# Kernel tuning notes

Hardware: AMD Instinct MI355X
Metric: run time of the kernel (lower is better)

## Reference

```python
import jax, jax.numpy as jnp
import numpy as np

NUM_HEADS = 12

def setup_inputs() -> dict:
    key = jax.random.key(0)
    ks = jax.random.split(key, 6)
    B, N, C, P = 16, 785, 768, 48
    return {
        "x": jax.random.normal(ks[0], (B, N, C), jnp.float32),
        "qkv_w": jax.random.normal(ks[1], (3 * C, C), jnp.float32) * 0.02,
        "pos_emb": jax.random.normal(ks[2], (N, N, P), jnp.float32) * 0.02,
        "pos_proj_w": jax.random.normal(ks[3], (NUM_HEADS, P), jnp.float32) * 0.02,
        "proj_w": jax.random.normal(ks[4], (C, C), jnp.float32) * 0.02,
        "proj_b": jnp.zeros((C,), jnp.float32),
    }

def reference(x, qkv_w, pos_emb, pos_proj_w, proj_w, proj_b):
    B, N, C = x.shape
    H = NUM_HEADS
    hd = C // H
    scale = hd ** -0.5
    # qkv projection: [B,N,3C] -> q,k,v each [B,H,N,hd]
    qkv = (x @ qkv_w.T).reshape(B, N, 3, H, hd)
    qkv = jnp.transpose(qkv, (2, 0, 3, 1, 4))
    q, k, v = qkv[0], qkv[1], qkv[2]
    # learned relative-position bias: [H,N,N]
    pos_score = jnp.einsum('nmp,hp->hnm', pos_emb, pos_proj_w)
    # attention scores: scale applied AFTER adding bias (matches original)
    attn = (jnp.einsum('bhnd,bhmd->bhnm', q, k) + pos_score[None]) * scale
    attn = jax.nn.softmax(attn, axis=-1)
    out = jnp.einsum('bhnm,bhmd->bhnd', attn, v)
    out = jnp.transpose(out, (0, 2, 1, 3)).reshape(B, N, C)
    return out @ proj_w.T + proj_b
```

## Files before the change

### kernel.cpp

```cpp
#include <hip/hip_runtime.h>
#include <hip/hip_fp16.h>

#define B_ 16
#define N_ 785
#define C_ 768
#define H_ 12
#define HD_ 64
#define P_ 48
#define M_ (B_*N_)
#define POSW 832
#define VTW  832
#define SLOG2E 0.1803368801111244f

#define OFF_Q   0
#define OFF_K   9646080
#define OFF_VT  19292160
#define OFF_POS 29515776
#define OFF_XF  37353216
#define OFF_AO  OFF_XF
#define OFF_WQ  47085312
#define OFF_WP  48854784

struct __align__(16) Half8 { __half h[8]; };
typedef _Float16 half8_t __attribute__((ext_vector_type(8)));
typedef _Float16 half4_t __attribute__((ext_vector_type(4)));
typedef float f32x4 __attribute__((ext_vector_type(4)));

__device__ __forceinline__ void gl16(const void* g, void* l) {
    __builtin_amdgcn_global_load_lds(
        (const __attribute__((address_space(1))) void*)g,
        (__attribute__((address_space(3))) void*)l, 16, 0, 0);
}

__device__ __forceinline__ int xcd_swz(int o, int nwg) {
    const int q = nwg >> 3, r = nwg & 7;
    const int xcd = o & 7, idx = o >> 3;
    const int base = xcd < r ? xcd * (q + 1) : r * (q + 1) + (xcd - r) * q;
    return base + idx;
}

#define NX4 2411520
#define NQ4 442368
#define NP4 147456
#define NTOT4 (NX4+NQ4+NP4)

__global__ __launch_bounds__(256) void convert_f16(
    const float* __restrict__ x, const float* __restrict__ wq,
    const float* __restrict__ wp, _Float16* __restrict__ xo,
    _Float16* __restrict__ wqo, _Float16* __restrict__ wpo)
{
    int i = blockIdx.x * 256 + threadIdx.x;
    const float4* s; _Float16* d; int o;
    if (i < NX4)            { s = (const float4*)x;  d = xo;  o = i; }
    else if (i < NX4 + NQ4) { s = (const float4*)wq; d = wqo; o = i - NX4; }
    else                    { s = (const float4*)wp; d = wpo; o = i - NX4 - NQ4; }
    float4 v = s[o];
    half4_t h = { (_Float16)v.x, (_Float16)v.y, (_Float16)v.z, (_Float16)v.w };
    *(half4_t*)&d[o * 4] = h;
}

#define QKV_NWG (18 * 99)

__global__ __launch_bounds__(256) void qkv_gemm_mfma(
    const _Float16* __restrict__ A, const _Float16* __restrict__ Bw,
    __half* __restrict__ qh, __half* __restrict__ kh, __half* __restrict__ vth)
{
    __shared__ _Float16 Asl[2][128 * 32];
    __shared__ _Float16 Bsl[2][128 * 32];

    const int t  = threadIdx.x;
    const int w  = t >> 6;
    const int l  = t & 63;
    const int lr = l & 15;
    const int lg = l >> 4;
    const int wm = (w >> 1) * 64;
    const int wn = (w & 1) * 64;

    const int g  = xcd_swz(blockIdx.x, QKV_NWG);
    const int nt = g % 18;
    const int n0 = nt * 128;
    const int m0 = (g / 18) * 128;

    const int f1 = t + 256;
    const int ar0 = t >> 2,  ac0 = (t & 3) * 8;
    const int ar1 = f1 >> 2, ac1 = (f1 & 3) * 8;
    const _Float16* Ag0 = A  + (size_t)(m0 + ar0) * 768 + ac0;
    const _Float16* Ag1 = A  + (size_t)(m0 + ar1) * 768 + ac1;
    const _Float16* Bg0 = Bw + (size_t)(n0 + ar0) * 768 + ac0;
    const _Float16* Bg1 = Bw + (size_t)(n0 + ar1) * 768 + ac1;

    f32x4 acc[4][4];
    #pragma unroll
    for (int i = 0; i < 4; ++i)
        #pragma unroll
        for (int j = 0; j < 4; ++j) acc[i][j] = (f32x4){0.f, 0.f, 0.f, 0.f};

    gl16(Ag0, &Asl[0][t * 8]); gl16(Ag1, &Asl[0][f1 * 8]);
    gl16(Bg0, &Bsl[0][t * 8]); gl16(Bg1, &Bsl[0][f1 * 8]);
    __syncthreads();

    #pragma unroll 2
    for (int it = 0; it < 24; ++it) {
        const int cur = it & 1;
        if (it < 23) {
            const int kn = (it + 1) * 32;
            gl16(Ag0 + kn, &Asl[cur ^ 1][t * 8]); gl16(Ag1 + kn, &Asl[cur ^ 1][f1 * 8]);
            gl16(Bg0 + kn, &Bsl[cur ^ 1][t * 8]); gl16(Bg1 + kn, &Bsl[cur ^ 1][f1 * 8]);
        }
        half8_t af[4], bf[4];
        #pragma unroll
        for (int i = 0; i < 4; ++i)
            af[i] = *(const half8_t*)&Asl[cur][(wm + i * 16 + lr) * 32 + lg * 8];
        #pragma unroll
        for (int j = 0; j < 4; ++j)
            bf[j] = *(const half8_t*)&Bsl[cur][(wn + j * 16 + lr) * 32 + lg * 8];
        __builtin_amdgcn_s_setprio(1);
        #pragma unroll
        for (int i = 0; i < 4; ++i)
            #pragma unroll
            for (int j = 0; j < 4; ++j)
                acc[i][j] = __builtin_amdgcn_mfma_f32_16x16x32_f16(af[i], bf[j], acc[i][j], 0, 0, 0);
        __builtin_amdgcn_s_setprio(0);
        __syncthreads();
    }

    const int tsel  = nt / 6;
    const int nbase = n0 - tsel * 768;
    #pragma unroll
    for (int i = 0; i < 4; ++i) {
        #pragma unroll
        for (int r = 0; r < 4; ++r) {
            const int m = m0 + wm + i * 16 + lg * 4 + r;
            if (m >= M_) continue;
            const int bb = m / N_, nn = m - bb * N_;
            #pragma unroll
            for (int j = 0; j < 4; ++j) {
                const int nsec = nbase + wn + j * 16 + lr;
                const int hh = nsec >> 6, dd = nsec & 63;
                const float v = acc[i][j][r];
                if (tsel == 0)
                    qh[((size_t)(bb * H_ + hh) * N_ + nn) * HD_ + dd] = __float2half(v * SLOG2E);
                else if (tsel == 1)
                    kh[((size_t)(bb * H_ + hh) * N_ + nn) * HD_ + dd] = __float2half(v);
                else
                    vth[((size_t)(bb * H_ + hh) * HD_ + dd) * VTW + nn] = __float2half(v);
            }
        }
    }
}

__global__ __launch_bounds__(256) void pos_kernel(
    const float* __restrict__ pe, const float* __restrict__ pw,
    __half* __restrict__ posh)
{
    __shared__ float W[H_][P_];
    const int t = threadIdx.x;
    for (int i = t; i < H_ * P_; i += 256) W[i / P_][i % P_] = pw[i];
    __syncthreads();
    int nm = blockIdx.x * 256 + t;
    if (nm >= N_ * N_) return;
    float e[48];
    const float4* src = (const float4*)(pe + (size_t)nm * 48);
    #pragma unroll
    for (int i = 0; i < 12; ++i) {
        float4 v = src[i];
        e[4*i] = v.x; e[4*i+1] = v.y; e[4*i+2] = v.z; e[4*i+3] = v.w;
    }
    int n = nm / N_, m = nm - n * N_;
    #pragma unroll
    for (int hh = 0; hh < H_; ++hh) {
        float s = 0.f;
        #pragma unroll
        for (int p = 0; p < 48; ++p) s = fmaf(e[p], W[hh][p], s);
        posh[((size_t)hh * N_ + n) * POSW + m] = __float2half(s * SLOG2E);
    }
}

__global__ __launch_bounds__(256) void attn_mfma(
    const _Float16* __restrict__ qh, const _Float16* __restrict__ kh,
    const _Float16* __restrict__ vt, const _Float16* __restrict__ posh,
    _Float16* __restrict__ aoh)
{
    __shared__ _Float16 Kl[64][72];
    __shared__ _Float16 Vl[64][72];
    __shared__ _Float16 Bl[64][72];

    const int t  = threadIdx.x;
    const int w  = t >> 6;
    const int l  = t & 63;
    const int lr = l & 15;
    const int lg = l >> 4;

    const int g   = blockIdx.x;
    const int b   = g & 15;
    const int grp = g >> 4;
    const int qt  = grp / 12;
    const int h   = grp - qt * 12;
    const int bh  = b * H_ + h;
    const int n0  = qt * 64;

    const int qrow = n0 + w * 16 + lr;
    const int qrc  = qrow < N_ ? qrow : N_ - 1;
    const _Float16* qbase = qh + ((size_t)bh * N_ + qrc) * HD_;
    const half8_t qf0 = *(const half8_t*)(qbase + lg * 8);
    const half8_t qf1 = *(const half8_t*)(qbase + 32 + lg * 8);

    f32x4 O0 = {0.f,0.f,0.f,0.f}, O1 = O0, O2 = O0, O3 = O0;
    float m_run = -1e30f;
    float l_run = 0.f;

    const int srow = t >> 2;
    const int scol = (t & 3) * 16;
    const _Float16* kRow = kh + ((size_t)bh * N_) * HD_ + scol;
    const _Float16* vRow = vt + ((size_t)bh * HD_ + srow) * VTW + scol;
    const _Float16* bRow = posh + ((size_t)h * N_ + (n0 + srow < N_ ? n0 + srow : N_ - 1)) * POSW + scol;

    half8_t rk0, rk1, rv0, rv1, rb0, rb1;
    {
        const int gm = srow < N_ ? srow : N_ - 1;
        const half8_t* ks = (const half8_t*)(kRow + (size_t)gm * HD_);
        rk0 = ks[0]; rk1 = ks[1];
        const half8_t* vs = (const half8_t*)vRow;
        rv0 = vs[0]; rv1 = vs[1];
        const half8_t* bs = (const half8_t*)bRow;
        rb0 = bs[0]; rb1 = bs[1];
    }

    for (int c = 0; c < 13; ++c) {
        *(half8_t*)&Kl[srow][scol]     = rk0;
        *(half8_t*)&Kl[srow][scol + 8] = rk1;
        *(half8_t*)&Vl[srow][scol]     = rv0;
        *(half8_t*)&Vl[srow][scol + 8] = rv1;
        *(half8_t*)&Bl[srow][scol]     = rb0;
        *(half8_t*)&Bl[srow][scol + 8] = rb1;
        __syncthreads();

        if (c < 12) {
            const int m0n = (c + 1) * 64;
            const int gm  = (m0n + srow) < N_ ? (m0n + srow) : N_ - 1;
            const half8_t* ks = (const half8_t*)(kRow + (size_t)gm * HD_);
            rk0 = ks[0]; rk1 = ks[1];
            const half8_t* vs = (const half8_t*)(vRow + m0n);
            rv0 = vs[0]; rv1 = vs[1];
            const half8_t* bs = (const half8_t*)(bRow + m0n);
            rb0 = bs[0]; rb1 = bs[1];
        }

        f32x4 s[4];
        __builtin_amdgcn_s_setprio(1);
        #pragma unroll
        for (int ms = 0; ms < 4; ++ms) {
            half8_t k0 = *(const half8_t*)&Kl[ms * 16 + lr][lg * 8];
            half8_t k1 = *(const half8_t*)&Kl[ms * 16 + lr][32 + lg * 8];
            f32x4 acc = {0.f, 0.f, 0.f, 0.f};
            acc = __builtin_amdgcn_mfma_f32_16x16x32_f16(k0, qf0, acc, 0, 0, 0);
            acc = __builtin_amdgcn_mfma_f32_16x16x32_f16(k1, qf1, acc, 0, 0, 0);
            s[ms] = acc;
        }
        __builtin_amdgcn_s_setprio(0);

        #pragma unroll
        for (int ms = 0; ms < 4; ++ms) {
            half4_t b4 = *(const half4_t*)&Bl[w * 16 + lr][ms * 16 + lg * 4];
            s[ms][0] += (float)b4[0];
            s[ms][1] += (float)b4[1];
            s[ms][2] += (float)b4[2];
            s[ms][3] += (float)b4[3];
        }
        if (c == 12) {
            #pragma unroll
            for (int ms = 0; ms < 4; ++ms)
                #pragma unroll
                for (int r = 0; r < 4; ++r)
                    if (ms * 16 + lg * 4 + r >= 17) s[ms][r] = -1e30f;
        }

        float smax = fmaxf(fmaxf(fmaxf(s[0][0], s[0][1]), fmaxf(s[0][2], s[0][3])),
                           fmaxf(fmaxf(s[1][0], s[1][1]), fmaxf(s[1][2], s[1][3])));
        smax = fmaxf(smax, fmaxf(fmaxf(fmaxf(s[2][0], s[2][1]), fmaxf(s[2][2], s[2][3])),
                                 fmaxf(fmaxf(s[3][0], s[3][1]), fmaxf(s[3][2], s[3][3]))));
        smax = fmaxf(smax, __shfl_xor(smax, 16));
        smax = fmaxf(smax, __shfl_xor(smax, 32));

        if (__any(smax > m_run + 8.f)) {
            const float mn    = fmaxf(m_run, smax);
            const float alpha = exp2f(m_run - mn);
            m_run = mn;
            l_run *= alpha;
            const float a0 = __shfl(alpha, lg * 4 + 0);
            const float a1 = __shfl(alpha, lg * 4 + 1);
            const float a2 = __shfl(alpha, lg * 4 + 2);
            const float a3 = __shfl(alpha, lg * 4 + 3);
            O0[0]*=a0; O0[1]*=a1; O0[2]*=a2; O0[3]*=a3;
            O1[0]*=a0; O1[1]*=a1; O1[2]*=a2; O1[3]*=a3;
            O2[0]*=a0; O2[1]*=a1; O2[2]*=a2; O2[3]*=a3;
            O3[0]*=a0; O3[1]*=a1; O3[2]*=a2; O3[3]*=a3;
        }

        float p[4][4];
        float psum = 0.f;
        #pragma unroll
        for (int ms = 0; ms < 4; ++ms)
            #pragma unroll
            for (int r = 0; r < 4; ++r) {
                p[ms][r] = exp2f(s[ms][r] - m_run);
                psum += p[ms][r];
            }
        psum += __shfl_xor(psum, 16);
        psum += __shfl_xor(psum, 32);
        l_run += psum;

        half8_t pa0 = { (_Float16)p[0][0], (_Float16)p[0][1], (_Float16)p[0][2], (_Float16)p[0][3],
                        (_Float16)p[1][0], (_Float16)p[1][1], (_Float16)p[1][2], (_Float16)p[1][3] };
        half8_t pa1 = { (_Float16)p[2][0], (_Float16)p[2][1], (_Float16)p[2][2], (_Float16)p[2][3],
                        (_Float16)p[3][0], (_Float16)p[3][1], (_Float16)p[3][2], (_Float16)p[3][3] };

        __builtin_amdgcn_s_setprio(1);
        #pragma unroll
        for (int ds = 0; ds < 4; ++ds) {
            const _Float16* vr = &Vl[ds * 16 + lr][0];
            half4_t v00 = *(const half4_t*)&vr[lg * 4];
            half4_t v01 = *(const half4_t*)&vr[16 + lg * 4];
            half4_t v10 = *(const half4_t*)&vr[32 + lg * 4];
            half4_t v11 = *(const half4_t*)&vr[48 + lg * 4];
            half8_t vf0 = __builtin_shufflevector(v00, v01, 0, 1, 2, 3, 4, 5, 6, 7);
            half8_t vf1 = __builtin_shufflevector(v10, v11, 0, 1, 2, 3, 4, 5, 6, 7);
            f32x4& Od = (ds == 0 ? O0 : ds == 1 ? O1 : ds == 2 ? O2 : O3);
            Od = __builtin_amdgcn_mfma_f32_16x16x32_f16(pa0, vf0, Od, 0, 0, 0);
            Od = __builtin_amdgcn_mfma_f32_16x16x32_f16(pa1, vf1, Od, 0, 0, 0);
        }
        __builtin_amdgcn_s_setprio(0);
        __syncthreads();
    }

    const int bb = bh / H_;
    #pragma unroll
    for (int r = 0; r < 4; ++r) {
        const int n = n0 + w * 16 + lg * 4 + r;
        if (n >= N_) continue;
        const float lv  = __shfl(l_run, lg * 4 + r);
        const float inv = 1.f / lv;
        _Float16* dst = aoh + ((size_t)(bb * N_ + n)) * C_ + h * HD_;
        dst[0 * 16 + lr] = (_Float16)(O0[r] * inv);
        dst[1 * 16 + lr] = (_Float16)(O1[r] * inv);
        dst[2 * 16 + lr] = (_Float16)(O2[r] * inv);
        dst[3 * 16 + lr] = (_Float16)(O3[r] * inv);
    }
}

#define PROJ_NWG (6 * 99)

__global__ __launch_bounds__(256) void proj_gemm_mfma(
    const _Float16* __restrict__ A, const _Float16* __restrict__ Bw,
    const float* __restrict__ bias, float* __restrict__ out)
{
    __shared__ _Float16 Asl[2][128 * 32];
    __shared__ _Float16 Bsl[2][128 * 32];

    const int t  = threadIdx.x;
    const int w  = t >> 6;
    const int l  = t & 63;
    const int lr = l & 15;
    const int lg = l >> 4;
    const int wm = (w >> 1) * 64;
    const int wn = (w & 1) * 64;

    const int g  = xcd_swz(blockIdx.x, PROJ_NWG);
    const int n0 = (g % 6) * 128;
    const int m0 = (g / 6) * 128;

    const int f1 = t + 256;
    const int ar0 = t >> 2,  ac0 = (t & 3) * 8;
    const int ar1 = f1 >> 2, ac1 = (f1 & 3) * 8;
    const _Float16* Ag0 = A  + (size_t)(m0 + ar0) * 768 + ac0;
    const _Float16* Ag1 = A  + (size_t)(m0 + ar1) * 768 + ac1;
    const _Float16* Bg0 = Bw + (size_t)(n0 + ar0) * 768 + ac0;
    const _Float16* Bg1 = Bw + (size_t)(n0 + ar1) * 768 + ac1;

    f32x4 acc[4][4];
    #pragma unroll
    for (int i = 0; i < 4; ++i)
        #pragma unroll
        for (int j = 0; j < 4; ++j) acc[i][j] = (f32x4){0.f, 0.f, 0.f, 0.f};

    gl16(Ag0, &Asl[0][t * 8]); gl16(Ag1, &Asl[0][f1 * 8]);
    gl16(Bg0, &Bsl[0][t * 8]); gl16(Bg1, &Bsl[0][f1 * 8]);
    __syncthreads();

    #pragma unroll 2
    for (int it = 0; it < 24; ++it) {
        const int cur = it & 1;
        if (it < 23) {
            const int kn = (it + 1) * 32;
            gl16(Ag0 + kn, &Asl[cur ^ 1][t * 8]); gl16(Ag1 + kn, &Asl[cur ^ 1][f1 * 8]);
            gl16(Bg0 + kn, &Bsl[cur ^ 1][t * 8]); gl16(Bg1 + kn, &Bsl[cur ^ 1][f1 * 8]);
        }
        half8_t af[4], bf[4];
        #pragma unroll
        for (int i = 0; i < 4; ++i)
            af[i] = *(const half8_t*)&Asl[cur][(wm + i * 16 + lr) * 32 + lg * 8];
        #pragma unroll
        for (int j = 0; j < 4; ++j)
            bf[j] = *(const half8_t*)&Bsl[cur][(wn + j * 16 + lr) * 32 + lg * 8];
        __builtin_amdgcn_s_setprio(1);
        #pragma unroll
        for (int i = 0; i < 4; ++i)
            #pragma unroll
            for (int j = 0; j < 4; ++j)
                acc[i][j] = __builtin_amdgcn_mfma_f32_16x16x32_f16(af[i], bf[j], acc[i][j], 0, 0, 0);
        __builtin_amdgcn_s_setprio(0);
        __syncthreads();
    }

    float bj[4];
    #pragma unroll
    for (int j = 0; j < 4; ++j) bj[j] = bias[n0 + wn + j * 16 + lr];
    #pragma unroll
    for (int i = 0; i < 4; ++i) {
        #pragma unroll
        for (int r = 0; r < 4; ++r) {
            const int m = m0 + wm + i * 16 + lg * 4 + r;
            if (m >= M_) continue;
            #pragma unroll
            for (int j = 0; j < 4; ++j) {
                const int n = n0 + wn + j * 16 + lr;
                out[(size_t)m * 768 + n] = acc[i][j][r] + bj[j];
            }
        }
    }
}

extern "C" void kernel_launch(void* const* d_in, const int* in_sizes, int n_in,
                              void* d_out, int out_size, void* d_ws, size_t ws_size,
                              hipStream_t stream)
{
    const float* x     = (const float*)d_in[0];
    const float* qkv_w = (const float*)d_in[1];
    const float* pe    = (const float*)d_in[2];
    const float* pw    = (const float*)d_in[3];
    const float* pjw   = (const float*)d_in[4];
    const float* pjb   = (const float*)d_in[5];
    float* out = (float*)d_out;

    _Float16* wsh  = (_Float16*)d_ws;
    _Float16* qh   = wsh + OFF_Q;
    _Float16* kh   = wsh + OFF_K;
    _Float16* vth  = wsh + OFF_VT;
    _Float16* posh = wsh + OFF_POS;
    _Float16* xf   = wsh + OFF_XF;
    _Float16* aoh  = wsh + OFF_AO;
    _Float16* wqf  = wsh + OFF_WQ;
    _Float16* wpf  = wsh + OFF_WP;

    convert_f16<<<dim3(NTOT4 / 256), 256, 0, stream>>>(x, qkv_w, pjw, xf, wqf, wpf);
    qkv_gemm_mfma<<<dim3(QKV_NWG), 256, 0, stream>>>(
        xf, wqf, (__half*)qh, (__half*)kh, (__half*)vth);
    pos_kernel<<<dim3((N_ * N_ + 255) / 256), 256, 0, stream>>>(pe, pw, (__half*)posh);
    attn_mfma<<<dim3(13 * 12 * 16), 256, 0, stream>>>(qh, kh, vth, posh, aoh);
    proj_gemm_mfma<<<dim3(PROJ_NWG), 256, 0, stream>>>(aoh, wpf, pjb, out);
}
```

Before: 270.1 us.

## Process 128 query rows per attention block to reuse K/V tiles

The attention kernel now assigns two 16-row query groups per wave, so each block covers 128 query rows instead of 64. Each K/V tile staged in shared memory feeds twice as many MFMAs, which halves K/V global traffic and the number of tile loads and barriers. Work-group indices are also remapped through an XCD swizzle so that blocks sharing a (b,h) land together. In exchange, register pressure and shared memory (a larger bias tile) go up, which may lower occupancy. Padding also grows, since the last of the 7 query tiles covers only 17 of its 128 rows.

```diff
diff --git a/kernel.cpp b/kernel.cpp
--- a/kernel.cpp
+++ b/kernel.cpp
@@ -176,6 +176,9 @@
     }
 }
 
+#define NQT 7
+#define ATT_NWG (192 * NQT)
+
 __global__ __launch_bounds__(256) void attn_mfma(
     const _Float16* __restrict__ qh, const _Float16* __restrict__ kh,
     const _Float16* __restrict__ vt, const _Float16* __restrict__ posh,
@@ -183,7 +186,7 @@
 {
     __shared__ _Float16 Kl[64][72];
     __shared__ _Float16 Vl[64][72];
-    __shared__ _Float16 Bl[64][72];
+    __shared__ _Float16 Bl[128][72];
 
     const int t  = threadIdx.x;
     const int w  = t >> 6;
@@ -191,129 +194,161 @@
     const int lr = l & 15;
     const int lg = l >> 4;
 
-    const int g   = blockIdx.x;
-    const int b   = g & 15;
-    const int grp = g >> 4;
-    const int qt  = grp / 12;
-    const int h   = grp - qt * 12;
-    const int bh  = b * H_ + h;
-    const int n0  = qt * 64;
-
-    const int qrow = n0 + w * 16 + lr;
-    const int qrc  = qrow < N_ ? qrow : N_ - 1;
-    const _Float16* qbase = qh + ((size_t)bh * N_ + qrc) * HD_;
-    const half8_t qf0 = *(const half8_t*)(qbase + lg * 8);
-    const half8_t qf1 = *(const half8_t*)(qbase + 32 + lg * 8);
-
-    f32x4 O0 = {0.f,0.f,0.f,0.f}, O1 = O0, O2 = O0, O3 = O0;
-    float m_run = -1e30f;
-    float l_run = 0.f;
+    const int g2   = xcd_swz(blockIdx.x, ATT_NWG);
+    const int qt   = g2 % NQT;
+    const int rest = g2 / NQT;
+    const int b    = rest & 15;
+    const int h    = rest >> 4;
+    const int bh   = b * H_ + h;
+    const int n0   = qt * 128;
+
+    const int qra = min(n0 + w * 32 + lr, N_ - 1);
+    const int qrb = min(n0 + w * 32 + 16 + lr, N_ - 1);
+    const _Float16* qpa = qh + ((size_t)bh * N_ + qra) * HD_;
+    const _Float16* qpb = qh + ((size_t)bh * N_ + qrb) * HD_;
+    const half8_t qf0a = *(const half8_t*)(qpa + lg * 8);
+    const half8_t qf1a = *(const half8_t*)(qpa + 32 + lg * 8);
+    const half8_t qf0b = *(const half8_t*)(qpb + lg * 8);
+    const half8_t qf1b = *(const half8_t*)(qpb + 32 + lg * 8);
+
+    f32x4 Oa0 = {0.f,0.f,0.f,0.f}, Oa1 = Oa0, Oa2 = Oa0, Oa3 = Oa0;
+    f32x4 Ob0 = Oa0, Ob1 = Oa0, Ob2 = Oa0, Ob3 = Oa0;
+    float ma = -1e30f, mb = -1e30f, la = 0.f, lb = 0.f;
 
     const int srow = t >> 2;
     const int scol = (t & 3) * 16;
-    const _Float16* kRow = kh + ((size_t)bh * N_) * HD_ + scol;
-    const _Float16* vRow = vt + ((size_t)bh * HD_ + srow) * VTW + scol;
-    const _Float16* bRow = posh + ((size_t)h * N_ + (n0 + srow < N_ ? n0 + srow : N_ - 1)) * POSW + scol;
-
-    half8_t rk0, rk1, rv0, rv1, rb0, rb1;
+    const _Float16* kRow  = kh + ((size_t)bh * N_) * HD_ + scol;
+    const _Float16* vRow  = vt + ((size_t)bh * HD_ + srow) * VTW + scol;
+    const _Float16* bRow0 = posh + ((size_t)h * N_ + min(n0 + srow,      N_ - 1)) * POSW + scol;
+    const _Float16* bRow1 = posh + ((size_t)h * N_ + min(n0 + 64 + srow, N_ - 1)) * POSW + scol;
+
+    half8_t rk0, rk1, rv0, rv1, rb0, rb1, rb2, rb3;
     {
-        const int gm = srow < N_ ? srow : N_ - 1;
+        const int gm = min(srow, N_ - 1);
         const half8_t* ks = (const half8_t*)(kRow + (size_t)gm * HD_);
         rk0 = ks[0]; rk1 = ks[1];
         const half8_t* vs = (const half8_t*)vRow;
         rv0 = vs[0]; rv1 = vs[1];
-        const half8_t* bs = (const half8_t*)bRow;
-        rb0 = bs[0]; rb1 = bs[1];
+        const half8_t* b0 = (const half8_t*)bRow0;
+        rb0 = b0[0]; rb1 = b0[1];
+        const half8_t* b1 = (const half8_t*)bRow1;
+        rb2 = b1[0]; rb3 = b1[1];
     }
 
     for (int c = 0; c < 13; ++c) {
-        *(half8_t*)&Kl[srow][scol]     = rk0;
-        *(half8_t*)&Kl[srow][scol + 8] = rk1;
-        *(half8_t*)&Vl[srow][scol]     = rv0;
-        *(half8_t*)&Vl[srow][scol + 8] = rv1;
-        *(half8_t*)&Bl[srow][scol]     = rb0;
-        *(half8_t*)&Bl[srow][scol + 8] = rb1;
+        *(half8_t*)&Kl[srow][scol]          = rk0;
+        *(half8_t*)&Kl[srow][scol + 8]      = rk1;
+        *(half8_t*)&Vl[srow][scol]          = rv0;
+        *(half8_t*)&Vl[srow][scol + 8]      = rv1;
+        *(half8_t*)&Bl[srow][scol]          = rb0;
+        *(half8_t*)&Bl[srow][scol + 8]      = rb1;
+        *(half8_t*)&Bl[64 + srow][scol]     = rb2;
+        *(half8_t*)&Bl[64 + srow][scol + 8] = rb3;
         __syncthreads();
 
         if (c < 12) {
             const int m0n = (c + 1) * 64;
-            const int gm  = (m0n + srow) < N_ ? (m0n + srow) : N_ - 1;
+            const int gm  = min(m0n + srow, N_ - 1);
             const half8_t* ks = (const half8_t*)(kRow + (size_t)gm * HD_);
             rk0 = ks[0]; rk1 = ks[1];
             const half8_t* vs = (const half8_t*)(vRow + m0n);
             rv0 = vs[0]; rv1 = vs[1];
-            const half8_t* bs = (const half8_t*)(bRow + m0n);
-            rb0 = bs[0]; rb1 = bs[1];
-        }
-
-        f32x4 s[4];
+            const half8_t* b0 = (const half8_t*)(bRow0 + m0n);
+            rb0 = b0[0]; rb1 = b0[1];
+            const half8_t* b1 = (const half8_t*)(bRow1 + m0n);
+            rb2 = b1[0]; rb3 = b1[1];
+        }
+
+        f32x4 sa[4], sb[4];
         __builtin_amdgcn_s_setprio(1);
         #pragma unroll
         for (int ms = 0; ms < 4; ++ms) {
             half8_t k0 = *(const half8_t*)&Kl[ms * 16 + lr][lg * 8];
             half8_t k1 = *(const half8_t*)&Kl[ms * 16 + lr][32 + lg * 8];
-            f32x4 acc = {0.f, 0.f, 0.f, 0.f};
-            acc = __builtin_amdgcn_mfma_f32_16x16x32_f16(k0, qf0, acc, 0, 0, 0);
-            acc = __builtin_amdgcn_mfma_f32_16x16x32_f16(k1, qf1, acc, 0, 0, 0);
-            s[ms] = acc;
+            f32x4 aa = {0.f, 0.f, 0.f, 0.f};
+            aa = __builtin_amdgcn_mfma_f32_16x16x32_f16(k0, qf0a, aa, 0, 0, 0);
+            aa = __builtin_amdgcn_mfma_f32_16x16x32_f16(k1, qf1a, aa, 0, 0, 0);
+            sa[ms] = aa;
+            f32x4 ab = {0.f, 0.f, 0.f, 0.f};
+            ab = __builtin_amdgcn_mfma_f32_16x16x32_f16(k0, qf0b, ab, 0, 0, 0);
+            ab = __builtin_amdgcn_mfma_f32_16x16x32_f16(k1, qf1b, ab, 0, 0, 0);
+            sb[ms] = ab;
         }
         __builtin_amdgcn_s_setprio(0);
 
         #pragma unroll
         for (int ms = 0; ms < 4; ++ms) {
-            half4_t b4 = *(const half4_t*)&Bl[w * 16 + lr][ms * 16 + lg * 4];
-            s[ms][0] += (float)b4[0];
-            s[ms][1] += (float)b4[1];
-            s[ms][2] += (float)b4[2];
-            s[ms][3] += (float)b4[3];
+            half4_t ba = *(const half4_t*)&Bl[w * 32 + lr][ms * 16 + lg * 4];
+            half4_t bbv = *(const half4_t*)&Bl[w * 32 + 16 + lr][ms * 16 + lg * 4];
+            #pragma unroll
+            for (int r = 0; r < 4; ++r) {
+                sa[ms][r] += (float)ba[r];
+                sb[ms][r] += (float)bbv[r];
+            }
         }
         if (c == 12) {
             #pragma unroll
             for (int ms = 0; ms < 4; ++ms)
                 #pragma unroll
                 for (int r = 0; r < 4; ++r)
-                    if (ms * 16 + lg * 4 + r >= 17) s[ms][r] = -1e30f;
-        }
-
-        float smax = fmaxf(fmaxf(fmaxf(s[0][0], s[0][1]), fmaxf(s[0][2], s[0][3])),
-                           fmaxf(fmaxf(s[1][0], s[1][1]), fmaxf(s[1][2], s[1][3])));
-        smax = fmaxf(smax, fmaxf(fmaxf(fmaxf(s[2][0], s[2][1]), fmaxf(s[2][2], s[2][3])),
-                                 fmaxf(fmaxf(s[3][0], s[3][1]), fmaxf(s[3][2], s[3][3]))));
-        smax = fmaxf(smax, __shfl_xor(smax, 16));
-        smax = fmaxf(smax, __shfl_xor(smax, 32));
-
-        if (__any(smax > m_run + 8.f)) {
-            const float mn    = fmaxf(m_run, smax);
-            const float alpha = exp2f(m_run - mn);
-            m_run = mn;
-            l_run *= alpha;
-            const float a0 = __shfl(alpha, lg * 4 + 0);
-            const float a1 = __shfl(alpha, lg * 4 + 1);
-            const float a2 = __shfl(alpha, lg * 4 + 2);
-            const float a3 = __shfl(alpha, lg * 4 + 3);
-            O0[0]*=a0; O0[1]*=a1; O0[2]*=a2; O0[3]*=a3;
-            O1[0]*=a0; O1[1]*=a1; O1[2]*=a2; O1[3]*=a3;
-            O2[0]*=a0; O2[1]*=a1; O2[2]*=a2; O2[3]*=a3;
-            O3[0]*=a0; O3[1]*=a1; O3[2]*=a2; O3[3]*=a3;
-        }
-
-        float p[4][4];
-        float psum = 0.f;
+                    if (ms * 16 + lg * 4 + r >= 17) { sa[ms][r] = -1e30f; sb[ms][r] = -1e30f; }
+        }
+
+        float sxa = fmaxf(fmaxf(fmaxf(sa[0][0], sa[0][1]), fmaxf(sa[0][2], sa[0][3])),
+                          fmaxf(fmaxf(sa[1][0], sa[1][1]), fmaxf(sa[1][2], sa[1][3])));
+        sxa = fmaxf(sxa, fmaxf(fmaxf(fmaxf(sa[2][0], sa[2][1]), fmaxf(sa[2][2], sa[2][3])),
+                               fmaxf(fmaxf(sa[3][0], sa[3][1]), fmaxf(sa[3][2], sa[3][3]))));
+        sxa = fmaxf(sxa, __shfl_xor(sxa, 16));
+        sxa = fmaxf(sxa, __shfl_xor(sxa, 32));
+        float sxb = fmaxf(fmaxf(fmaxf(sb[0][0], sb[0][1]), fmaxf(sb[0][2], sb[0][3])),
+                          fmaxf(fmaxf(sb[1][0], sb[1][1]), fmaxf(sb[1][2], sb[1][3])));
+        sxb = fmaxf(sxb, fmaxf(fmaxf(fmaxf(sb[2][0], sb[2][1]), fmaxf(sb[2][2], sb[2][3])),
+                               fmaxf(fmaxf(sb[3][0], sb[3][1]), fmaxf(sb[3][2], sb[3][3]))));
+        sxb = fmaxf(sxb, __shfl_xor(sxb, 16));
+        sxb = fmaxf(sxb, __shfl_xor(sxb, 32));
+
+        if (__any(fmaxf(sxa - ma, sxb - mb) > 8.f)) {
+            const float mna = fmaxf(ma, sxa);
+            const float ala = exp2f(ma - mna);
+            ma = mna; la *= ala;
+            const float mnb = fmaxf(mb, sxb);
+            const float alb = exp2f(mb - mnb);
+            mb = mnb; lb *= alb;
+            #pragma unroll
+            for (int r = 0; r < 4; ++r) {
+                const float ar = __shfl(ala, lg * 4 + r);
+                Oa0[r] *= ar; Oa1[r] *= ar; Oa2[r] *= ar; Oa3[r] *= ar;
+                const float br = __shfl(alb, lg * 4 + r);
+                Ob0[r] *= br; Ob1[r] *= br; Ob2[r] *= br; Ob3[r] *= br;
+            }
+        }
+
+        float pa[4][4], pb[4][4];
+        float psa = 0.f, psb = 0.f;
         #pragma unroll
         for (int ms = 0; ms < 4; ++ms)
             #pragma unroll
             for (int r = 0; r < 4; ++r) {
-                p[ms][r] = exp2f(s[ms][r] - m_run);
-                psum += p[ms][r];
+                pa[ms][r] = exp2f(sa[ms][r] - ma);
+                psa += pa[ms][r];
+                pb[ms][r] = exp2f(sb[ms][r] - mb);
+                psb += pb[ms][r];
             }
-        psum += __shfl_xor(psum, 16);
-        psum += __shfl_xor(psum, 32);
-        l_run += psum;
-
-        half8_t pa0 = { (_Float16)p[0][0], (_Float16)p[0][1], (_Float16)p[0][2], (_Float16)p[0][3],
-                        (_Float16)p[1][0], (_Float16)p[1][1], (_Float16)p[1][2], (_Float16)p[1][3] };
-        half8_t pa1 = { (_Float16)p[2][0], (_Float16)p[2][1], (_Float16)p[2][2], (_Float16)p[2][3],
-                        (_Float16)p[3][0], (_Float16)p[3][1], (_Float16)p[3][2], (_Float16)p[3][3] };
+        psa += __shfl_xor(psa, 16);
+        psa += __shfl_xor(psa, 32);
+        la += psa;
+        psb += __shfl_xor(psb, 16);
+        psb += __shfl_xor(psb, 32);
+        lb += psb;
+
+        half8_t paf0 = { (_Float16)pa[0][0], (_Float16)pa[0][1], (_Float16)pa[0][2], (_Float16)pa[0][3],
+                         (_Float16)pa[1][0], (_Float16)pa[1][1], (_Float16)pa[1][2], (_Float16)pa[1][3] };
+        half8_t paf1 = { (_Float16)pa[2][0], (_Float16)pa[2][1], (_Float16)pa[2][2], (_Float16)pa[2][3],
+                         (_Float16)pa[3][0], (_Float16)pa[3][1], (_Float16)pa[3][2], (_Float16)pa[3][3] };
+        half8_t pbf0 = { (_Float16)pb[0][0], (_Float16)pb[0][1], (_Float16)pb[0][2], (_Float16)pb[0][3],
+                         (_Float16)pb[1][0], (_Float16)pb[1][1], (_Float16)pb[1][2], (_Float16)pb[1][3] };
+        half8_t pbf1 = { (_Float16)pb[2][0], (_Float16)pb[2][1], (_Float16)pb[2][2], (_Float16)pb[2][3],
+                         (_Float16)pb[3][0], (_Float16)pb[3][1], (_Float16)pb[3][2], (_Float16)pb[3][3] };
 
         __builtin_amdgcn_s_setprio(1);
         #pragma unroll
@@ -325,9 +360,12 @@
             half4_t v11 = *(const half4_t*)&vr[48 + lg * 4];
             half8_t vf0 = __builtin_shufflevector(v00, v01, 0, 1, 2, 3, 4, 5, 6, 7);
             half8_t vf1 = __builtin_shufflevector(v10, v11, 0, 1, 2, 3, 4, 5, 6, 7);
-            f32x4& Od = (ds == 0 ? O0 : ds == 1 ? O1 : ds == 2 ? O2 : O3);
-            Od = __builtin_amdgcn_mfma_f32_16x16x32_f16(pa0, vf0, Od, 0, 0, 0);
-            Od = __builtin_amdgcn_mfma_f32_16x16x32_f16(pa1, vf1, Od, 0, 0, 0);
+            f32x4& Oda = (ds == 0 ? Oa0 : ds == 1 ? Oa1 : ds == 2 ? Oa2 : Oa3);
+            Oda = __builtin_amdgcn_mfma_f32_16x16x32_f16(paf0, vf0, Oda, 0, 0, 0);
+            Oda = __builtin_amdgcn_mfma_f32_16x16x32_f16(paf1, vf1, Oda, 0, 0, 0);
+            f32x4& Odb = (ds == 0 ? Ob0 : ds == 1 ? Ob1 : ds == 2 ? Ob2 : Ob3);
+            Odb = __builtin_amdgcn_mfma_f32_16x16x32_f16(pbf0, vf0, Odb, 0, 0, 0);
+            Odb = __builtin_amdgcn_mfma_f32_16x16x32_f16(pbf1, vf1, Odb, 0, 0, 0);
         }
         __builtin_amdgcn_s_setprio(0);
         __syncthreads();
@@ -336,15 +374,26 @@
     const int bb = bh / H_;
     #pragma unroll
     for (int r = 0; r < 4; ++r) {
-        const int n = n0 + w * 16 + lg * 4 + r;
-        if (n >= N_) continue;
-        const float lv  = __shfl(l_run, lg * 4 + r);
-        const float inv = 1.f / lv;
-        _Float16* dst = aoh + ((size_t)(bb * N_ + n)) * C_ + h * HD_;
-        dst[0 * 16 + lr] = (_Float16)(O0[r] * inv);
-        dst[1 * 16 + lr] = (_Float16)(O1[r] * inv);
-        dst[2 * 16 + lr] = (_Float16)(O2[r] * inv);
-        dst[3 * 16 + lr] = (_Float16)(O3[r] * inv);
+        const int na = n0 + w * 32 + lg * 4 + r;
+        if (na < N_) {
+            const float lv  = __shfl(la, lg * 4 + r);
+            const float inv = 1.f / lv;
+            _Float16* dst = aoh + ((size_t)(bb * N_ + na)) * C_ + h * HD_;
+            dst[0 * 16 + lr] = (_Float16)(Oa0[r] * inv);
+            dst[1 * 16 + lr] = (_Float16)(Oa1[r] * inv);
+            dst[2 * 16 + lr] = (_Float16)(Oa2[r] * inv);
+            dst[3 * 16 + lr] = (_Float16)(Oa3[r] * inv);
+        }
+        const int nb = na + 16;
+        if (nb < N_) {
+            const float lv  = __shfl(lb, lg * 4 + r);
+            const float inv = 1.f / lv;
+            _Float16* dst = aoh + ((size_t)(bb * N_ + nb)) * C_ + h * HD_;
+            dst[0 * 16 + lr] = (_Float16)(Ob0[r] * inv);
+            dst[1 * 16 + lr] = (_Float16)(Ob1[r] * inv);
+            dst[2 * 16 + lr] = (_Float16)(Ob2[r] * inv);
+            dst[3 * 16 + lr] = (_Float16)(Ob3[r] * inv);
+        }
     }
 }
 
@@ -456,6 +505,6 @@
     qkv_gemm_mfma<<<dim3(QKV_NWG), 256, 0, stream>>>(
         xf, wqf, (__half*)qh, (__half*)kh, (__half*)vth);
     pos_kernel<<<dim3((N_ * N_ + 255) / 256), 256, 0, stream>>>(pe, pw, (__half*)posh);
-    attn_mfma<<<dim3(13 * 12 * 16), 256, 0, stream>>>(qh, kh, vth, posh, aoh);
+    attn_mfma<<<dim3(ATT_NWG), 256, 0, stream>>>(qh, kh, vth, posh, aoh);
     proj_gemm_mfma<<<dim3(PROJ_NWG), 256, 0, stream>>>(aoh, wpf, pjb, out);
 }
```

Result: slower. 278.3 us (+3.0%).
